# Kernel tuning notes

Hardware: AMD Instinct MI355X
Metric: run time of the kernel (lower is better)

Reference implementation:

```python
import jax, jax.numpy as jnp
import numpy as np

N, F_IN, HID, CLUST = 4096, 128, 128, 128
HEADS = 2
RADIUS = 2.0
TOPK_ADD = 2
MOTIF_TOPK = 8
ETA = 0.5
L0_GAMMA, L0_ZETA = -0.1, 1.1
NEG_SLOPE = 0.2
BN_EPS = 1e-5
NEG_INF = -1e9


def _row_topk(A, k):
    # keep top-k per row, symmetrize by max, zero diagonal (matches row_topk)
    n = A.shape[0]
    if n <= k:
        S = A
    else:
        vals, idx = jax.lax.top_k(A, k)
        S = jnp.zeros_like(A).at[jnp.arange(n)[:, None], idx].set(vals)
        S = jnp.maximum(S, S.T)
    return S * (1.0 - jnp.eye(n, dtype=A.dtype))


def _bn_eval(x, g, b, m, v):
    return (x - m) * g * jax.lax.rsqrt(v + BN_EPS) + b


def _gate(logits, tau):
    # hard-concrete gate, eval path
    t = jnp.clip(tau, 0.1, None)
    s = jax.nn.sigmoid(logits / t) * (L0_ZETA - L0_GAMMA) + L0_GAMMA
    return jnp.clip(s, 0.0, 1.0)


def _gcn_dense(feat, A_w, W, b):
    # GCN: D^-1/2 A D^-1/2 (X W) + b, zero-degree rows -> 0
    deg = A_w.sum(axis=1)
    dinv = jnp.where(deg > 0, jax.lax.rsqrt(jnp.where(deg > 0, deg, 1.0)), 0.0)
    An = dinv[:, None] * A_w * dinv[None, :]
    return An @ (feat @ W) + b


def setup_inputs():
    key = jax.random.key(0)
    ks = jax.random.split(key, 30)
    eye = jnp.eye(N, dtype=jnp.float32)
    p = 16.0 / N  # ~16 avg degree
    B = jax.random.uniform(ks[0], (N, N)) < p
    A_in = ((B | B.T) & ~jnp.eye(N, dtype=bool)).astype(jnp.float32)
    Mw = jnp.where(jax.random.uniform(ks[1], (N, N)) < p, jax.random.uniform(ks[2], (N, N)), 0.0)
    A_motif = jnp.maximum(Mw, Mw.T) * (1.0 - eye)
    coords = jax.random.randint(ks[3], (N, 2), 0, 64).astype(jnp.float32)
    x = jax.random.normal(ks[4], (N, F_IN))
    s_in = 1.0 / np.sqrt(F_IN)
    s_h = 1.0 / np.sqrt(2 * HID)
    return {
        'x': x, 'A_in': A_in, 'A_motif': A_motif, 'coords': coords,
        'gat_w': jax.random.normal(ks[5], (F_IN, HEADS * HID)) * s_in,
        'gat_asrc': jax.random.normal(ks[6], (HEADS, HID)) * s_h,
        'gat_adst': jax.random.normal(ks[7], (HEADS, HID)) * s_h,
        'gat_b': jnp.zeros((HEADS * HID,)),
        'bnA_g': jnp.ones((2 * HID,)), 'bnA_b': jnp.zeros((2 * HID,)),
        'bnA_m': jax.random.normal(ks[8], (2 * HID,)) * 0.1,
        'bnA_v': 0.5 + jax.random.uniform(ks[9], (2 * HID,)),
        'gcnM_w': jax.random.normal(ks[10], (F_IN, 2 * HID)) * s_in,
        'gcnM_b': jnp.zeros((2 * HID,)),
        'bnM_g': jnp.ones((2 * HID,)), 'bnM_b': jnp.zeros((2 * HID,)),
        'bnM_m': jax.random.normal(ks[11], (2 * HID,)) * 0.1,
        'bnM_v': 0.5 + jax.random.uniform(ks[12], (2 * HID,)),
        'mu': jnp.asarray(-3.0), 'tau': jnp.asarray(1.0),
        'prune_w': jax.random.normal(ks[13], (4 * HID + 1,)) * s_h,
        'prune_b': jnp.asarray(0.0),
        'rewire_w': jax.random.normal(ks[14], (4 * HID + 1,)) * s_h,
        'rewire_b': jnp.asarray(0.0),
        'pool_w': jax.random.normal(ks[15], (2 * HID, CLUST)) * s_h,
        'pool_b': jnp.zeros((CLUST,)),
    }


def reference(x, A_in, A_motif, coords, gat_w, gat_asrc, gat_adst, gat_b,
              bnA_g, bnA_b, bnA_m, bnA_v, gcnM_w, gcnM_b, bnM_g, bnM_b, bnM_m, bnM_v,
              mu, tau, prune_w, prune_b, rewire_w, rewire_b, pool_w, pool_b):
    n = x.shape[0]
    eye = jnp.eye(n, dtype=x.dtype)
    # --- GAT branch on A_in (dense masked attention; PyG adds self loops) ---
    Wx = (x @ gat_w).reshape(n, HEADS, HID)           # [N, heads, H]
    a_src = (Wx * gat_asrc).sum(-1)                   # [N, heads]
    a_dst = (Wx * gat_adst).sum(-1)
    e = jax.nn.leaky_relu(a_dst[:, None, :] + a_src[None, :, :], NEG_SLOPE)  # e[i,j,h]
    adj_mask = (A_in > 0) | jnp.eye(n, dtype=bool)
    e = jnp.where(adj_mask[..., None], e, NEG_INF)
    alpha = jax.nn.softmax(e, axis=1)                 # softmax over sources j
    h_A = jnp.einsum('ijh,jhd->ihd', alpha, Wx).reshape(n, HEADS * HID) + gat_b
    h_A = jax.nn.elu(_bn_eval(h_A, bnA_g, bnA_b, bnA_m, bnA_v))
    # --- motif branch ---
    M_hat = _row_topk(A_motif, MOTIF_TOPK)
    h_M = jax.nn.elu(_bn_eval(_gcn_dense(x, M_hat, gcnM_w, gcnM_b), bnM_g, bnM_b, bnM_m, bnM_v))
    h = h_A + jax.nn.softplus(mu) * h_M               # [N, 2H]
    d2 = 2 * HID
    triu = jnp.triu(jnp.ones((n, n), dtype=bool), 1)
    # --- prune gate on existing upper-tri edges (Linear is separable) ---
    pu = h @ prune_w[:d2]
    pv = h @ prune_w[d2:2 * d2]
    prune_logits = pu[:, None] + pv[None, :] + prune_w[2 * d2] * M_hat + prune_b
    z_prune = _gate(prune_logits, tau)
    edge_u = triu & (A_in > 0)
    Wp = jnp.where(edge_u, z_prune * A_in, 0.0)
    A_pruned = Wp + Wp.T
    # --- rewire candidates: L1 cdist within radius, non-edges, upper tri ---
    dist = jnp.abs(coords[:, None, :] - coords[None, :, :]).sum(-1)
    cand_u = (dist > 0) & (dist <= RADIUS) & (A_in < 1e-6) & triu
    ru = h @ rewire_w[:d2]
    rv = h @ rewire_w[d2:2 * d2]
    rew_logits = ru[:, None] + rv[None, :] + rewire_w[2 * d2] * M_hat + rewire_b
    Zu = jnp.where(cand_u, _gate(rew_logits, tau), 0.0)
    # per-node top-k selection over incident candidates (symmetric view)
    cand_sym = cand_u | cand_u.T
    scores = jnp.where(cand_sym, Zu + Zu.T, NEG_INF)
    thr = jax.lax.top_k(scores, TOPK_ADD)[0][:, -1]
    keep = (scores >= thr[:, None]) & cand_sym
    pair_keep = (keep | keep.T) & cand_u
    A_added_u = jnp.where(pair_keep, Zu, 0.0)
    A_added_sym = jnp.maximum(A_added_u, A_added_u.T)
    A_refined = A_pruned + ETA * A_added_sym
    # --- pooling GCN (default GCNConv adds self loops, weight 1) ---
    S = jax.nn.softmax(_gcn_dense(h, A_refined + eye, pool_w, pool_b), axis=1)  # [N, C]
    X_coarse = S.T @ h                                 # [C, 2H]
    A_c = S.T @ A_refined @ S
    A_c = A_c * (1.0 - jnp.eye(A_c.shape[0], dtype=A_c.dtype))
    A_coarse = _row_topk(A_c, MOTIF_TOPK)
    return X_coarse, A_coarse
```

## Files before the change

kernel.cpp:

```cpp
#include <hip/hip_runtime.h>
#include <hip/hip_bf16.h>
#include <stdint.h>

#define N 4096
#define FIN 128
#define HID 128
#define D2 256
#define CLUST 128
#define NEG_INF (-1e9f)
#define KAJ 128
#define KM 96
#define KC 64
#define KA (KAJ + KC)
#define CCAP 32
#define JCH 128
#define NCH (N/JCH)
#define CTILE 16
#define POSCAP 256

typedef __hip_bfloat16 bf16;

__device__ __forceinline__ float cvt(float v){ return v; }
__device__ __forceinline__ float cvt(bf16 v){ return __bfloat162float(v); }
__device__ __forceinline__ void stout(float* p, size_t i, float v){ p[i] = v; }
__device__ __forceinline__ void stout(bf16* p, size_t i, float v){ p[i] = __float2bfloat16(v); }

__device__ __forceinline__ float hc_gate(float l, float tau){
  float t = fmaxf(tau, 0.1f);
  float s = 1.f / (1.f + expf(-l / t));
  s = s * 1.2f - 0.1f;
  return fminf(fmaxf(s, 0.f), 1.f);
}

__global__ void k_detect(const void* x, const void* w, int* flag, int* cellCnt){
  __shared__ int hits;
  int t = threadIdx.x;
  if (t == 0) hits = 0;
  for (int i = t; i < 4096; i += 256) cellCnt[i] = 0;
  __syncthreads();
  const bf16* xb = (const bf16*)x;
  const bf16* wb = (const bf16*)w;
  int h = 0;
  for (int i = t; i < 2048; i += 256){
    float a = __bfloat162float(xb[i]);
    float b = __bfloat162float(wb[i]);
    if (!(fabsf(a) < 1e6f)) ++h;
    if (!(fabsf(b) < 1e6f)) ++h;
  }
  atomicAdd(&hits, h);
  __syncthreads();
  if (t == 0) *flag = (hits > 0) ? 1 : 0;
}

template<typename T>
__device__ void xw2_body(const T* x, const T* gat_w, const T* gcnM_w,
                         float* Wx, float* xwM, float* xr){
  int i0 = blockIdx.x * 4, t = threadIdx.x;
  for (int idx = t; idx < 4*FIN; idx += 256) xr[idx] = cvt(x[(size_t)i0*FIN + idx]);
  __syncthreads();
  float wx[4], xm[4];
  #pragma unroll
  for (int r = 0; r < 4; ++r){ wx[r] = 0.f; xm[r] = 0.f; }
  #pragma unroll 4
  for (int k = 0; k < FIN; ++k){
    float wa = cvt(gat_w[k*D2 + t]);
    float wm = cvt(gcnM_w[k*D2 + t]);
    #pragma unroll
    for (int r = 0; r < 4; ++r){
      wx[r] += xr[r*FIN + k] * wa;
      xm[r] += xr[r*FIN + k] * wm;
    }
  }
  #pragma unroll
  for (int r = 0; r < 4; ++r){
    Wx[(size_t)(i0+r)*D2 + t] = wx[r];
    xwM[(size_t)(i0+r)*D2 + t] = xm[r];
  }
}
__global__ void k_xw2(const int* fl, const void* x, const void* gw, const void* gmw,
                      float* Wx, float* xwM){
  __shared__ float xr[4*FIN];
  if (*fl) xw2_body<float>((const float*)x,(const float*)gw,(const float*)gmw,Wx,xwM,xr);
  else     xw2_body<bf16 >((const bf16*)x,(const bf16*)gw,(const bf16*)gmw,Wx,xwM,xr);
}

template<typename T>
__device__ void att_body(const float* Wx, const T* asrc, const T* adst,
                         float* a_src, float* a_dst){
  int w = threadIdx.x >> 6, l = threadIdx.x & 63;
  int row = blockIdx.x*4 + w;
  const float4* wr = (const float4*)(Wx + (size_t)row*D2);
  float4 v = wr[l];
  float s0 = cvt(asrc[l*4])*v.x + cvt(asrc[l*4+1])*v.y
           + cvt(asrc[l*4+2])*v.z + cvt(asrc[l*4+3])*v.w;
  float s1 = cvt(adst[l*4])*v.x + cvt(adst[l*4+1])*v.y
           + cvt(adst[l*4+2])*v.z + cvt(adst[l*4+3])*v.w;
  for (int d = 16; d > 0; d >>= 1){
    s0 += __shfl_down(s0, d, 32);
    s1 += __shfl_down(s1, d, 32);
  }
  if ((l & 31) == 0){
    a_src[row*2 + (l >> 5)] = s0;
    a_dst[row*2 + (l >> 5)] = s1;
  }
}
__global__ void k_att(const int* fl, const float* Wx, const void* as, const void* ad,
                      float* a_src, float* a_dst){
  if (*fl) att_body<float>(Wx,(const float*)as,(const float*)ad,a_src,a_dst);
  else     att_body<bf16 >(Wx,(const bf16*)as,(const bf16*)ad,a_src,a_dst);
}

__device__ __forceinline__ void t8_insert(unsigned long long* keys, float v, int j){
  unsigned long long key =
    ((unsigned long long)__float_as_uint(v) << 32) | (unsigned int)(~(unsigned int)j);
  if (key > keys[7]){
    keys[7] = key;
    #pragma unroll
    for (int q = 7; q > 0; --q){
      if (keys[q] > keys[q-1]){ unsigned long long tmp = keys[q]; keys[q] = keys[q-1]; keys[q-1] = tmp; }
    }
  }
}
__global__ void k_top8(const int* fl, const void* Amot, float* t8v, int* t8i,
                       int* Midx, float* Mval, int* Mcnt){
  __shared__ int pj[POSCAP];
  __shared__ float pv[POSCAP];
  __shared__ int cnt;
  int i = blockIdx.x, t = threadIdx.x;
  if (t == 0) cnt = 0;
  __syncthreads();
  if (*fl){
    const float4* rowp = (const float4*)((const float*)Amot + (size_t)i*N);
    for (int s = 0; s < N/1024; ++s){
      float4 v4 = rowp[s*256 + t];
      int jb = s*1024 + t*4;
      if (v4.x > 0.f){ int p = atomicAdd(&cnt,1); if (p < POSCAP){ pj[p] = jb;   pv[p] = v4.x; } }
      if (v4.y > 0.f){ int p = atomicAdd(&cnt,1); if (p < POSCAP){ pj[p] = jb+1; pv[p] = v4.y; } }
      if (v4.z > 0.f){ int p = atomicAdd(&cnt,1); if (p < POSCAP){ pj[p] = jb+2; pv[p] = v4.z; } }
      if (v4.w > 0.f){ int p = atomicAdd(&cnt,1); if (p < POSCAP){ pj[p] = jb+3; pv[p] = v4.w; } }
    }
  } else {
    const bf16* rowp = (const bf16*)Amot + (size_t)i*N;
    for (int j = t; j < N; j += 256){
      float v = cvt(rowp[j]);
      if (v > 0.f){ int p = atomicAdd(&cnt,1); if (p < POSCAP){ pj[p] = j; pv[p] = v; } }
    }
  }
  __syncthreads();
  if (t == 0){
    int n = min(cnt, POSCAP);
    unsigned long long keys[8];
    #pragma unroll
    for (int q = 0; q < 8; ++q) keys[q] = 0ull;
    for (int e = 0; e < n; ++e) t8_insert(keys, pv[e], pj[e]);
    int c = 0;
    #pragma unroll
    for (int r = 0; r < 8; ++r){
      float v = __uint_as_float((unsigned int)(keys[r] >> 32));
      int j = (int)(~(unsigned int)keys[r]);
      bool ok = (keys[r] != 0ull) && (v > 0.f);
      t8v[i*8 + r] = ok ? v : 0.f;
      t8i[i*8 + r] = ok ? j : -1;
      if (ok){ Midx[i*KM + c] = j; Mval[i*KM + c] = v; ++c; }
    }
    Mcnt[i] = c;
  }
}

__global__ void k_mscat(const float* __restrict__ t8v, const int* __restrict__ t8i,
                        int* __restrict__ Midx, float* __restrict__ Mval,
                        int* __restrict__ Mcnt){
  int e = blockIdx.x*256 + threadIdx.x;
  if (e >= N*8) return;
  int i = e >> 3;
  int j = t8i[e];
  if (j < 0) return;
  #pragma unroll
  for (int s = 0; s < 8; ++s) if (t8i[j*8 + s] == i) return;
  int p = atomicAdd(&Mcnt[j], 1);
  if (p < KM){ Midx[j*KM + p] = i; Mval[j*KM + p] = t8v[e]; }
}

__global__ void k_degM(const float* __restrict__ Mval, const int* __restrict__ Mcnt,
                       float* __restrict__ dinvM){
  int i = blockIdx.x*256 + threadIdx.x;
  if (i >= N) return;
  int n = min(Mcnt[i], KM);
  float s = 0.f;
  for (int e = 0; e < n; ++e) s += Mval[i*KM + e];
  dinvM[i] = (s > 0.f) ? rsqrtf(s) : 0.f;
}

template<typename T>
__device__ void motif_body(const int* Midx, const float* Mval, const int* Mcnt,
                           const float* dinvM, const float* xwM, const T* gcnM_b,
                           const T* bng, const T* bnb, const T* bnm, const T* bnv,
                           float* hM, int* nj, float* nw){
  int i = blockIdx.x, t = threadIdx.x;
  int n = min(Mcnt[i], KM);
  for (int e = t; e < n; e += 256){
    int j = Midx[i*KM + e];
    nj[e] = j;
    nw[e] = Mval[i*KM + e] * dinvM[j];
  }
  __syncthreads();
  float a0 = 0.f, a1 = 0.f, a2 = 0.f, a3 = 0.f;
  int e = 0;
  for (; e + 3 < n; e += 4){
    a0 += nw[e]   * xwM[nj[e]*D2 + t];
    a1 += nw[e+1] * xwM[nj[e+1]*D2 + t];
    a2 += nw[e+2] * xwM[nj[e+2]*D2 + t];
    a3 += nw[e+3] * xwM[nj[e+3]*D2 + t];
  }
  for (; e < n; ++e) a0 += nw[e] * xwM[nj[e]*D2 + t];
  float acc = (a0 + a1) + (a2 + a3);
  float val = acc * dinvM[i] + cvt(gcnM_b[t]);
  val = (val - cvt(bnm[t])) * cvt(bng[t]) * rsqrtf(cvt(bnv[t]) + 1e-5f) + cvt(bnb[t]);
  val = (val > 0.f) ? val : expm1f(val);
  hM[i*D2 + t] = val;
}
__global__ void k_motif_agg(const int* fl, const int* Midx, const float* Mval,
                            const int* Mcnt, const float* dinvM, const float* xwM,
                            const void* gb, const void* g, const void* b,
                            const void* m, const void* v, float* hM){
  __shared__ int nj[KM];
  __shared__ float nw[KM];
  if (*fl) motif_body<float>(Midx,Mval,Mcnt,dinvM,xwM,(const float*)gb,(const float*)g,
                             (const float*)b,(const float*)m,(const float*)v,hM,nj,nw);
  else     motif_body<bf16 >(Midx,Mval,Mcnt,dinvM,xwM,(const bf16*)gb,(const bf16*)g,
                             (const bf16*)b,(const bf16*)m,(const bf16*)v,hM,nj,nw);
}

__global__ void k_adj(const int* fl, const void* Ain,
                      int* __restrict__ AdjIdx, float* __restrict__ AdjVal,
                      int* __restrict__ AdjCnt){
  __shared__ int cnt;
  int i = blockIdx.x, t = threadIdx.x;
  if (t == 0) cnt = 0;
  __syncthreads();
  if (*fl){
    const float4* rowp = (const float4*)((const float*)Ain + (size_t)i*N);
    for (int s = 0; s < N/1024; ++s){
      float4 v4 = rowp[s*256 + t];
      int jb = s*1024 + t*4;
      if (v4.x > 0.f && jb   != i){ int p = atomicAdd(&cnt,1); if (p < KAJ){ AdjIdx[i*KAJ+p] = jb;   AdjVal[i*KAJ+p] = v4.x; } }
      if (v4.y > 0.f && jb+1 != i){ int p = atomicAdd(&cnt,1); if (p < KAJ){ AdjIdx[i*KAJ+p] = jb+1; AdjVal[i*KAJ+p] = v4.y; } }
      if (v4.z > 0.f && jb+2 != i){ int p = atomicAdd(&cnt,1); if (p < KAJ){ AdjIdx[i*KAJ+p] = jb+2; AdjVal[i*KAJ+p] = v4.z; } }
      if (v4.w > 0.f && jb+3 != i){ int p = atomicAdd(&cnt,1); if (p < KAJ){ AdjIdx[i*KAJ+p] = jb+3; AdjVal[i*KAJ+p] = v4.w; } }
    }
  } else {
    const bf16* rowp = (const bf16*)Ain + (size_t)i*N;
    for (int j = t; j < N; j += 256){
      float v = cvt(rowp[j]);
      if (v > 0.f && j != i){ int p = atomicAdd(&cnt,1); if (p < KAJ){ AdjIdx[i*KAJ+p] = j; AdjVal[i*KAJ+p] = v; } }
    }
  }
  __syncthreads();
  if (t == 0) AdjCnt[i] = min(cnt, KAJ);
}

template<typename T>
__device__ void gat_body(const int* AdjIdx, const int* AdjCnt, const float* Wx,
                         const float* a_src, const float* a_dst, const T* gat_b,
                         const T* bng, const T* bnb, const T* bnm, const T* bnv,
                         const float* hM, const T* mu,
                         float* h, int* nbr, float* ew, float* mm, float* inv){
  int i = blockIdx.x, t = threadIdx.x;
  int na = AdjCnt[i];
  for (int e = t; e < na; e += 256) nbr[e] = AdjIdx[i*KAJ + e];
  if (t == 0) nbr[na] = i;
  __syncthreads();
  int n = na + 1;
  float ad0 = a_dst[i*2], ad1 = a_dst[i*2 + 1];
  for (int e = t; e < n; e += 256){
    int j = nbr[e];
    float e0 = ad0 + a_src[j*2];
    float e1 = ad1 + a_src[j*2 + 1];
    e0 = (e0 > 0.f) ? e0 : 0.2f * e0;
    e1 = (e1 > 0.f) ? e1 : 0.2f * e1;
    ew[2*e] = e0; ew[2*e + 1] = e1;
  }
  __syncthreads();
  if (t == 0){
    float m0 = -3.4e38f, m1 = -3.4e38f;
    for (int e = 0; e < n; ++e){ m0 = fmaxf(m0, ew[2*e]); m1 = fmaxf(m1, ew[2*e+1]); }
    mm[0] = m0; mm[1] = m1;
  }
  __syncthreads();
  for (int e = t; e < n; e += 256){
    ew[2*e]   = expf(ew[2*e]   - mm[0]);
    ew[2*e+1] = expf(ew[2*e+1] - mm[1]);
  }
  __syncthreads();
  if (t == 0){
    float s0 = 0.f, s1 = 0.f;
    for (int e = 0; e < n; ++e){ s0 += ew[2*e]; s1 += ew[2*e+1]; }
    inv[0] = 1.f/s0; inv[1] = 1.f/s1;
  }
  __syncthreads();
  int hh = t >> 7;
  float a0 = 0.f, a1 = 0.f, a2 = 0.f, a3 = 0.f;
  int e = 0;
  for (; e + 3 < n; e += 4){
    a0 += ew[2*e + hh]     * Wx[nbr[e]*D2 + t];
    a1 += ew[2*(e+1) + hh] * Wx[nbr[e+1]*D2 + t];
    a2 += ew[2*(e+2) + hh] * Wx[nbr[e+2]*D2 + t];
    a3 += ew[2*(e+3) + hh] * Wx[nbr[e+3]*D2 + t];
  }
  for (; e < n; ++e) a0 += ew[2*e + hh] * Wx[nbr[e]*D2 + t];
  float acc = (a0 + a1) + (a2 + a3);
  float val = acc * inv[hh] + cvt(gat_b[t]);
  val = (val - cvt(bnm[t])) * cvt(bng[t]) * rsqrtf(cvt(bnv[t]) + 1e-5f) + cvt(bnb[t]);
  val = (val > 0.f) ? val : expm1f(val);
  float spmu = log1pf(expf(cvt(mu[0])));
  h[i*D2 + t] = val + spmu * hM[i*D2 + t];
}
__global__ void k_gat_agg(const int* fl, const int* AdjIdx, const int* AdjCnt,
                          const float* Wx, const float* a_src, const float* a_dst,
                          const void* gb, const void* g, const void* b, const void* m,
                          const void* v, const float* hM, const void* mu, float* h){
  __shared__ int nbr[KAJ + 1];
  __shared__ float ew[(KAJ + 1)*2];
  __shared__ float mm[2], inv[2];
  if (*fl) gat_body<float>(AdjIdx,AdjCnt,Wx,a_src,a_dst,(const float*)gb,(const float*)g,
                           (const float*)b,(const float*)m,(const float*)v,hM,(const float*)mu,
                           h,nbr,ew,mm,inv);
  else     gat_body<bf16 >(AdjIdx,AdjCnt,Wx,a_src,a_dst,(const bf16*)gb,(const bf16*)g,
                           (const bf16*)b,(const bf16*)m,(const bf16*)v,hM,(const bf16*)mu,
                           h,nbr,ew,mm,inv);
}

template<typename T>
__device__ void puv_body(const float* h, const T* pw, const T* rw,
                         float* pu, float* pv, float* ru, float* rv, float* red){
  int i = blockIdx.x, t = threadIdx.x;
  float hv = h[i*D2 + t];
  float v0 = hv * cvt(pw[t]);
  float v1 = hv * cvt(pw[D2 + t]);
  float v2 = hv * cvt(rw[t]);
  float v3 = hv * cvt(rw[D2 + t]);
  red[t] = v0; __syncthreads();
  for (int k = 128; k > 0; k >>= 1){ if (t < k) red[t] += red[t+k]; __syncthreads(); }
  if (t == 0) pu[i] = red[0];
  __syncthreads();
  red[t] = v1; __syncthreads();
  for (int k = 128; k > 0; k >>= 1){ if (t < k) red[t] += red[t+k]; __syncthreads(); }
  if (t == 0) pv[i] = red[0];
  __syncthreads();
  red[t] = v2; __syncthreads();
  for (int k = 128; k > 0; k >>= 1){ if (t < k) red[t] += red[t+k]; __syncthreads(); }
  if (t == 0) ru[i] = red[0];
  __syncthreads();
  red[t] = v3; __syncthreads();
  for (int k = 128; k > 0; k >>= 1){ if (t < k) red[t] += red[t+k]; __syncthreads(); }
  if (t == 0) rv[i] = red[0];
}
__global__ void k_puv(const int* fl, const float* h, const void* pw, const void* rw,
                      float* pu, float* pv, float* ru, float* rv){
  __shared__ float red[256];
  if (*fl) puv_body<float>(h,(const float*)pw,(const float*)rw,pu,pv,ru,rv,red);
  else     puv_body<bf16 >(h,(const bf16*)pw,(const bf16*)rw,pu,pv,ru,rv,red);
}

template<typename T>
__device__ void gridb_body(const T* coords, int* cellCnt, int* cellNode){
  int i = blockIdx.x*256 + threadIdx.x;
  if (i >= N) return;
  int cx = (int)cvt(coords[2*i]), cy = (int)cvt(coords[2*i+1]);
  int cell = cy*64 + cx;
  int p = atomicAdd(&cellCnt[cell], 1);
  if (p < CCAP) cellNode[cell*CCAP + p] = i;
}
__global__ void k_gridb(const int* fl, const void* coords, int* cellCnt, int* cellNode){
  if (*fl) gridb_body<float>((const float*)coords, cellCnt, cellNode);
  else     gridb_body<bf16 >((const bf16*)coords, cellCnt, cellNode);
}

template<typename T>
__device__ void cand_body(const T* coords, const T* Ain,
                          const int* Midx, const float* Mval, const int* Mcnt,
                          const int* cellCnt, const int* cellNode,
                          const float* ru, const float* rv,
                          const T* rw, const T* rb, const T* taup,
                          int* Cidx, float* Cz, int* Ccnt, float* thr,
                          int* scI, float* scZ, int* scn){
  int w = threadIdx.x >> 6, l = threadIdx.x & 63;
  int i = blockIdx.x*4 + w;
  if (l == 0) scn[w] = 0;
  __syncthreads();
  float cix = cvt(coords[2*i]), ciy = cvt(coords[2*i+1]);
// ... 230 lines not shown
    float acc[CTILE];
    #pragma unroll
    for (int cc = 0; cc < CTILE; ++cc) acc[cc] = 0.f;
    for (int j = 0; j < JCH; ++j){
      float v = T_[(size_t)(j0 + j)*CLUST + tt];
      #pragma unroll
      for (int cc = 0; cc < CTILE; ++cc) acc[cc] += ss[j][cc] * v;
    }
    #pragma unroll
    for (int cc = 0; cc < CTILE; ++cc)
      PA[((size_t)ch*CLUST + c0 + cc)*CLUST + tt] = acc[cc];
  }
}

template<typename OT>
__device__ void coarse2_body(const float* PX, const float* PA, OT* Xout, float* Ac){
  int c = blockIdx.x, t = threadIdx.x;
  if (t < 256){
    float s = 0.f;
    #pragma unroll 8
    for (int ch = 0; ch < NCH; ++ch) s += PX[((size_t)ch*CLUST + c)*D2 + t];
    stout(Xout, (size_t)c*D2 + t, s);
  } else {
    int tt = t - 256;
    float s = 0.f;
    #pragma unroll 8
    for (int ch = 0; ch < NCH; ++ch) s += PA[((size_t)ch*CLUST + c)*CLUST + tt];
    Ac[c*CLUST + tt] = (tt == c) ? 0.f : s;
  }
}
__global__ void k_coarse2(const int* fl, const float* PX, const float* PA,
                          void* out, float* Ac){
  if (*fl) coarse2_body<float>(PX, PA, (float*)out, Ac);
  else     coarse2_body<bf16 >(PX, PA, (bf16*)out, Ac);
}

__global__ void k_top8c(const float* __restrict__ Ac, float* __restrict__ Acs){
  __shared__ unsigned long long red[128];
  int r = blockIdx.x, t = threadIdx.x;
  float v = Ac[r*CLUST + t];
  unsigned long long mykey =
    ((unsigned long long)__float_as_uint(fmaxf(v, 0.f)) << 32) | (unsigned int)(~(unsigned int)t);
  unsigned long long last = ~0ull;
  bool selected = false;
  for (int q = 0; q < 8; ++q){
    red[t] = (mykey < last) ? mykey : 0ull;
    __syncthreads();
    for (int k = 64; k > 0; k >>= 1){
      if (t < k){ if (red[t+k] > red[t]) red[t] = red[t+k]; }
      __syncthreads();
    }
    unsigned long long win = red[0];
    __syncthreads();
    if (win != 0ull && win == mykey) selected = true;
    last = win;
  }
  Acs[r*CLUST + t] = (selected && v > 0.f) ? v : 0.f;
}

template<typename OT>
__device__ void sym_body(const float* Acs, OT* out){
  int r = blockIdx.x, t = threadIdx.x;
  float v = (r == t) ? 0.f : fmaxf(Acs[r*CLUST + t], Acs[t*CLUST + r]);
  stout(out, (size_t)(CLUST*D2) + r*CLUST + t, v);
}
__global__ void k_sym(const int* fl, const float* Acs, void* out){
  if (*fl) sym_body<float>(Acs, (float*)out);
  else     sym_body<bf16 >(Acs, (bf16*)out);
}

extern "C" void kernel_launch(void* const* d_in, const int* in_sizes, int n_in,
                              void* d_out, int out_size, void* d_ws, size_t ws_size,
// ... 31 lines not shown
    void* r = (void*)p;
    p += (bytes + 255) & ~(size_t)255;
    return r;
  };
  int*   flag    = (int*)  alloc(256);
  float* Wx      = (float*)alloc((size_t)N*D2*4);
  float* xwM     = (float*)alloc((size_t)N*D2*4);
  float* a_src   = (float*)alloc((size_t)N*2*4);
  float* a_dst   = (float*)alloc((size_t)N*2*4);
  float* t8v     = (float*)alloc((size_t)N*8*4);
  int*   t8i     = (int*)  alloc((size_t)N*8*4);
  int*   Midx    = (int*)  alloc((size_t)N*KM*4);
  float* Mval    = (float*)alloc((size_t)N*KM*4);
  int*   Mcnt    = (int*)  alloc((size_t)N*4);
  float* dinvM   = (float*)alloc((size_t)N*4);
  float* hM      = (float*)alloc((size_t)N*D2*4);
  float* hbuf    = (float*)alloc((size_t)N*D2*4);
  float* pu      = (float*)alloc((size_t)N*4);
  float* pv      = (float*)alloc((size_t)N*4);
  float* ru      = (float*)alloc((size_t)N*4);
  float* rv      = (float*)alloc((size_t)N*4);
  int*   AdjIdx  = (int*)  alloc((size_t)N*KAJ*4);
  float* AdjVal  = (float*)alloc((size_t)N*KAJ*4);
  int*   AdjCnt  = (int*)  alloc((size_t)N*4);
  int*   cellCnt = (int*)  alloc((size_t)4096*4);
  int*   cellNode= (int*)  alloc((size_t)4096*CCAP*4);
  int*   Cidx    = (int*)  alloc((size_t)N*KC*4);
  float* Cz      = (float*)alloc((size_t)N*KC*4);
  int*   Ccnt    = (int*)  alloc((size_t)N*4);
  float* thr     = (float*)alloc((size_t)N*4);
  int*   Aidx    = (int*)  alloc((size_t)N*KA*4);
  float* Aval    = (float*)alloc((size_t)N*KA*4);
  int*   Acnt    = (int*)  alloc((size_t)N*4);
  float* dinvR   = (float*)alloc((size_t)N*4);
  float* hW      = (float*)alloc((size_t)N*CLUST*4);
  float* S       = (float*)alloc((size_t)N*CLUST*4);
  float* T       = (float*)alloc((size_t)N*CLUST*4);
  float* PX      = (float*)alloc((size_t)NCH*CLUST*D2*4);
  float* PA      = (float*)alloc((size_t)NCH*CLUST*CLUST*4);
  float* Ac      = (float*)alloc((size_t)CLUST*CLUST*4);
  float* Acs     = (float*)alloc((size_t)CLUST*CLUST*4);

  k_detect<<<1, 256, 0, stream>>>(x, gat_w, flag, cellCnt);
  k_xw2<<<N/4, 256, 0, stream>>>(flag, x, gat_w, gcnM_w, Wx, xwM);
  k_att<<<N/4, 256, 0, stream>>>(flag, Wx, gat_asrc, gat_adst, a_src, a_dst);
  k_top8<<<N, 256, 0, stream>>>(flag, A_motif, t8v, t8i, Midx, Mval, Mcnt);
  k_mscat<<<(N*8)/256, 256, 0, stream>>>(t8v, t8i, Midx, Mval, Mcnt);
  k_degM<<<N/256, 256, 0, stream>>>(Mval, Mcnt, dinvM);
  k_motif_agg<<<N, 256, 0, stream>>>(flag, Midx, Mval, Mcnt, dinvM, xwM, gcnM_b,
                                     bnM_g, bnM_b, bnM_m, bnM_v, hM);
  k_adj<<<N, 256, 0, stream>>>(flag, A_in, AdjIdx, AdjVal, AdjCnt);
  k_gridb<<<16, 256, 0, stream>>>(flag, coords, cellCnt, cellNode);
  k_gat_agg<<<N, 256, 0, stream>>>(flag, AdjIdx, AdjCnt, Wx, a_src, a_dst, gat_b,
                                   bnA_g, bnA_b, bnA_m, bnA_v, hM, mu, hbuf);
  k_puv<<<N, 256, 0, stream>>>(flag, hbuf, prune_w, rewire_w, pu, pv, ru, rv);
  k_cand<<<N/4, 256, 0, stream>>>(flag, coords, A_in, Midx, Mval, Mcnt, cellCnt, cellNode,
                                  ru, rv, rewire_w, rewire_b, tau, Cidx, Cz, Ccnt, thr);
  k_aref<<<N/4, 256, 0, stream>>>(flag, AdjIdx, AdjVal, AdjCnt, Midx, Mval, Mcnt,
                                  pu, pv, prune_w, prune_b, tau, Cidx, Cz, Ccnt, thr,
                                  Aidx, Aval, Acnt, dinvR);
  k_hw<<<N/8, 128, 0, stream>>>(flag, hbuf, pool_w, hW);
  k_preS<<<N, 256, 0, stream>>>(flag, Aidx, Aval, Acnt, dinvR, hW, pool_b, S);
  k_T<<<N, 256, 0, stream>>>(Aidx, Aval, Acnt, S, T);
  k_coarse1<<<dim3(CLUST/CTILE, NCH), 384, 0, stream>>>(S, hbuf, T, PX, PA);
  k_coarse2<<<CLUST, 384, 0, stream>>>(flag, PX, PA, d_out, Ac);
  k_top8c<<<CLUST, 128, 0, stream>>>(Ac, Acs);
  k_sym<<<CLUST, 128, 0, stream>>>(flag, Acs, d_out);
}
```

Baseline: 404.1 us.

## Fuse kernels: xw2+att, motif/adj/grid scans, motif+GAT+puv aggregation, coarse2+top8

Merges several small launches into larger kernels. The attention dot products are computed from shared memory inside the x@W kernel, and the A_motif and A_in row scans plus grid bucketing share one pass per row. The motif GCN, GAT aggregation and prune/rewire projections run in one per-node kernel, which drops the hM intermediate buffer. The coarse top-8 selection moves into k_coarse2 as a serial insertion by one thread. This cuts launch overhead and global round-trips, at the cost of larger per-block work and a serial top-8 on a single thread.

```diff
diff --git a/kernel.cpp b/kernel.cpp
--- a/kernel.cpp
+++ b/kernel.cpp
@@ -32,6 +32,18 @@
   return fminf(fmaxf(s, 0.f), 1.f);
 }
 
+__device__ __forceinline__ void t8_insert(unsigned long long* keys, float v, int j){
+  unsigned long long key =
+    ((unsigned long long)__float_as_uint(v) << 32) | (unsigned int)(~(unsigned int)j);
+  if (key > keys[7]){
+    keys[7] = key;
+    #pragma unroll
+    for (int q = 7; q > 0; --q){
+      if (keys[q] > keys[q-1]){ unsigned long long tmp = keys[q]; keys[q] = keys[q-1]; keys[q-1] = tmp; }
+    }
+  }
+}
+
 __global__ void k_detect(const void* x, const void* w, int* flag, int* cellCnt){
   __shared__ int hits;
   int t = threadIdx.x;
@@ -54,9 +66,11 @@
 
 template<typename T>
 __device__ void xw2_body(const T* x, const T* gat_w, const T* gcnM_w,
-                         float* Wx, float* xwM, float* xr){
+                         const T* asrc, const T* adst,
+                         float* Wx, float* xwM, float* a_src, float* a_dst,
+                         float* sh){
   int i0 = blockIdx.x * 4, t = threadIdx.x;
-  for (int idx = t; idx < 4*FIN; idx += 256) xr[idx] = cvt(x[(size_t)i0*FIN + idx]);
+  for (int idx = t; idx < 4*FIN; idx += 256) sh[idx] = cvt(x[(size_t)i0*FIN + idx]);
   __syncthreads();
   float wx[4], xm[4];
   #pragma unroll
@@ -67,8 +81,8 @@
     float wm = cvt(gcnM_w[k*D2 + t]);
     #pragma unroll
     for (int r = 0; r < 4; ++r){
-      wx[r] += xr[r*FIN + k] * wa;
-      xm[r] += xr[r*FIN + k] * wm;
+      wx[r] += sh[r*FIN + k] * wa;
+      xm[r] += sh[r*FIN + k] * wm;
     }
   }
   #pragma unroll
@@ -76,21 +90,13 @@
     Wx[(size_t)(i0+r)*D2 + t] = wx[r];
     xwM[(size_t)(i0+r)*D2 + t] = xm[r];
   }
-}
-__global__ void k_xw2(const int* fl, const void* x, const void* gw, const void* gmw,
-                      float* Wx, float* xwM){
-  __shared__ float xr[4*FIN];
-  if (*fl) xw2_body<float>((const float*)x,(const float*)gw,(const float*)gmw,Wx,xwM,xr);
-  else     xw2_body<bf16 >((const bf16*)x,(const bf16*)gw,(const bf16*)gmw,Wx,xwM,xr);
-}
-
-template<typename T>
-__device__ void att_body(const float* Wx, const T* asrc, const T* adst,
-                         float* a_src, float* a_dst){
-  int w = threadIdx.x >> 6, l = threadIdx.x & 63;
-  int row = blockIdx.x*4 + w;
-  const float4* wr = (const float4*)(Wx + (size_t)row*D2);
-  float4 v = wr[l];
+  __syncthreads();
+  #pragma unroll
+  for (int r = 0; r < 4; ++r) sh[r*256 + t] = wx[r];
+  __syncthreads();
+  int w = t >> 6, l = t & 63;
+  int row = i0 + w;
+  float4 v = ((const float4*)(sh + w*256))[l];
   float s0 = cvt(asrc[l*4])*v.x + cvt(asrc[l*4+1])*v.y
            + cvt(asrc[l*4+2])*v.z + cvt(asrc[l*4+3])*v.w;
   float s1 = cvt(adst[l*4])*v.x + cvt(adst[l*4+1])*v.y
@@ -104,51 +110,52 @@
     a_dst[row*2 + (l >> 5)] = s1;
   }
 }
-__global__ void k_att(const int* fl, const float* Wx, const void* as, const void* ad,
-                      float* a_src, float* a_dst){
-  if (*fl) att_body<float>(Wx,(const float*)as,(const float*)ad,a_src,a_dst);
-  else     att_body<bf16 >(Wx,(const bf16*)as,(const bf16*)ad,a_src,a_dst);
-}
-
-__device__ __forceinline__ void t8_insert(unsigned long long* keys, float v, int j){
-  unsigned long long key =
-    ((unsigned long long)__float_as_uint(v) << 32) | (unsigned int)(~(unsigned int)j);
-  if (key > keys[7]){
-    keys[7] = key;
-    #pragma unroll
-    for (int q = 7; q > 0; --q){
-      if (keys[q] > keys[q-1]){ unsigned long long tmp = keys[q]; keys[q] = keys[q-1]; keys[q-1] = tmp; }
-    }
-  }
-}
-__global__ void k_top8(const int* fl, const void* Amot, float* t8v, int* t8i,
-                       int* Midx, float* Mval, int* Mcnt){
-  __shared__ int pj[POSCAP];
-  __shared__ float pv[POSCAP];
-  __shared__ int cnt;
+__global__ void k_xw2(const int* fl, const void* x, const void* gw, const void* gmw,
+                      const void* as, const void* ad,
+                      float* Wx, float* xwM, float* a_src, float* a_dst){
+  __shared__ float sh[1024];
+  if (*fl) xw2_body<float>((const float*)x,(const float*)gw,(const float*)gmw,
+                           (const float*)as,(const float*)ad,Wx,xwM,a_src,a_dst,sh);
+  else     xw2_body<bf16 >((const bf16*)x,(const bf16*)gw,(const bf16*)gmw,
+                           (const bf16*)as,(const bf16*)ad,Wx,xwM,a_src,a_dst,sh);
+}
+
+template<typename T>
+__device__ void scan_body(const T* Amot, const T* Ain, const T* coords,
+                          float* t8v, int* t8i, int* Midx, float* Mval, int* Mcnt,
+                          int* AdjIdx, float* AdjVal, int* AdjCnt,
+                          int* cellCnt, int* cellNode,
+                          int* pj, float* pv, int* cntM, int* cntA){
   int i = blockIdx.x, t = threadIdx.x;
-  if (t == 0) cnt = 0;
-  __syncthreads();
-  if (*fl){
-    const float4* rowp = (const float4*)((const float*)Amot + (size_t)i*N);
-    for (int s = 0; s < N/1024; ++s){
-      float4 v4 = rowp[s*256 + t];
-      int jb = s*1024 + t*4;
-      if (v4.x > 0.f){ int p = atomicAdd(&cnt,1); if (p < POSCAP){ pj[p] = jb;   pv[p] = v4.x; } }
-      if (v4.y > 0.f){ int p = atomicAdd(&cnt,1); if (p < POSCAP){ pj[p] = jb+1; pv[p] = v4.y; } }
-      if (v4.z > 0.f){ int p = atomicAdd(&cnt,1); if (p < POSCAP){ pj[p] = jb+2; pv[p] = v4.z; } }
-      if (v4.w > 0.f){ int p = atomicAdd(&cnt,1); if (p < POSCAP){ pj[p] = jb+3; pv[p] = v4.w; } }
-    }
-  } else {
-    const bf16* rowp = (const bf16*)Amot + (size_t)i*N;
+  if (t == 0){
+    *cntM = 0; *cntA = 0;
+    int cx = (int)cvt(coords[2*i]), cy = (int)cvt(coords[2*i+1]);
+    int cell = cy*64 + cx;
+    int p = atomicAdd(&cellCnt[cell], 1);
+    if (p < CCAP) cellNode[cell*CCAP + p] = i;
+  }
+  __syncthreads();
+  {
+    const T* rowp = Amot + (size_t)i*N;
     for (int j = t; j < N; j += 256){
       float v = cvt(rowp[j]);
-      if (v > 0.f){ int p = atomicAdd(&cnt,1); if (p < POSCAP){ pj[p] = j; pv[p] = v; } }
+      if (v > 0.f){ int p = atomicAdd(cntM,1); if (p < POSCAP){ pj[p] = j; pv[p] = v; } }
+    }
+  }
+  {
+    const T* rowp = Ain + (size_t)i*N;
+    for (int j = t; j < N; j += 256){
+      float v = cvt(rowp[j]);
+      if (v > 0.f && j != i){
+        int p = atomicAdd(cntA,1);
+        if (p < KAJ){ AdjIdx[i*KAJ+p] = j; AdjVal[i*KAJ+p] = v; }
+      }
     }
   }
   __syncthreads();
   if (t == 0){
-    int n = min(cnt, POSCAP);
+    AdjCnt[i] = min(*cntA, KAJ);
+    int n = min(*cntM, POSCAP);
     unsigned long long keys[8];
     #pragma unroll
     for (int q = 0; q < 8; ++q) keys[q] = 0ull;
@@ -165,6 +172,77 @@
     }
     Mcnt[i] = c;
   }
+}
+__device__ void scan_body_f4(const float* Amot, const float* Ain, const float* coords,
+                             float* t8v, int* t8i, int* Midx, float* Mval, int* Mcnt,
+                             int* AdjIdx, float* AdjVal, int* AdjCnt,
+                             int* cellCnt, int* cellNode,
+                             int* pj, float* pv, int* cntM, int* cntA){
+  int i = blockIdx.x, t = threadIdx.x;
+  if (t == 0){
+    *cntM = 0; *cntA = 0;
+    int cx = (int)coords[2*i], cy = (int)coords[2*i+1];
+    int cell = cy*64 + cx;
+    int p = atomicAdd(&cellCnt[cell], 1);
+    if (p < CCAP) cellNode[cell*CCAP + p] = i;
+  }
+  __syncthreads();
+  {
+    const float4* rowp = (const float4*)(Amot + (size_t)i*N);
+    for (int s = 0; s < N/1024; ++s){
+      float4 v4 = rowp[s*256 + t];
+      int jb = s*1024 + t*4;
+      if (v4.x > 0.f){ int p = atomicAdd(cntM,1); if (p < POSCAP){ pj[p] = jb;   pv[p] = v4.x; } }
+      if (v4.y > 0.f){ int p = atomicAdd(cntM,1); if (p < POSCAP){ pj[p] = jb+1; pv[p] = v4.y; } }
+      if (v4.z > 0.f){ int p = atomicAdd(cntM,1); if (p < POSCAP){ pj[p] = jb+2; pv[p] = v4.z; } }
+      if (v4.w > 0.f){ int p = atomicAdd(cntM,1); if (p < POSCAP){ pj[p] = jb+3; pv[p] = v4.w; } }
+    }
+  }
+  {
+    const float4* rowp = (const float4*)(Ain + (size_t)i*N);
+    for (int s = 0; s < N/1024; ++s){
+      float4 v4 = rowp[s*256 + t];
+      int jb = s*1024 + t*4;
+      if (v4.x > 0.f && jb   != i){ int p = atomicAdd(cntA,1); if (p < KAJ){ AdjIdx[i*KAJ+p] = jb;   AdjVal[i*KAJ+p] = v4.x; } }
+      if (v4.y > 0.f && jb+1 != i){ int p = atomicAdd(cntA,1); if (p < KAJ){ AdjIdx[i*KAJ+p] = jb+1; AdjVal[i*KAJ+p] = v4.y; } }
+      if (v4.z > 0.f && jb+2 != i){ int p = atomicAdd(cntA,1); if (p < KAJ){ AdjIdx[i*KAJ+p] = jb+2; AdjVal[i*KAJ+p] = v4.z; } }
+      if (v4.w > 0.f && jb+3 != i){ int p = atomicAdd(cntA,1); if (p < KAJ){ AdjIdx[i*KAJ+p] = jb+3; AdjVal[i*KAJ+p] = v4.w; } }
+    }
+  }
+  __syncthreads();
+  if (t == 0){
+    AdjCnt[i] = min(*cntA, KAJ);
+    int n = min(*cntM, POSCAP);
+    unsigned long long keys[8];
+    #pragma unroll
+    for (int q = 0; q < 8; ++q) keys[q] = 0ull;
+    for (int e = 0; e < n; ++e) t8_insert(keys, pv[e], pj[e]);
+    int c = 0;
+    #pragma unroll
+    for (int r = 0; r < 8; ++r){
+      float v = __uint_as_float((unsigned int)(keys[r] >> 32));
+      int j = (int)(~(unsigned int)keys[r]);
+      bool ok = (keys[r] != 0ull) && (v > 0.f);
+      t8v[i*8 + r] = ok ? v : 0.f;
+      t8i[i*8 + r] = ok ? j : -1;
+      if (ok){ Midx[i*KM + c] = j; Mval[i*KM + c] = v; ++c; }
+    }
+    Mcnt[i] = c;
+  }
+}
+__global__ void k_scan(const int* fl, const void* Amot, const void* Ain, const void* coords,
+                       float* t8v, int* t8i, int* Midx, float* Mval, int* Mcnt,
+                       int* AdjIdx, float* AdjVal, int* AdjCnt,
+                       int* cellCnt, int* cellNode){
+  __shared__ int pj[POSCAP];
+  __shared__ float pv[POSCAP];
+  __shared__ int cntM, cntA;
+  if (*fl) scan_body_f4((const float*)Amot,(const float*)Ain,(const float*)coords,
+                        t8v,t8i,Midx,Mval,Mcnt,AdjIdx,AdjVal,AdjCnt,cellCnt,cellNode,
+                        pj,pv,&cntM,&cntA);
+  else     scan_body<bf16>((const bf16*)Amot,(const bf16*)Ain,(const bf16*)coords,
+                        t8v,t8i,Midx,Mval,Mcnt,AdjIdx,AdjVal,AdjCnt,cellCnt,cellNode,
+                        pj,pv,&cntM,&cntA);
 }
 
 __global__ void k_mscat(const float* __restrict__ t8v, const int* __restrict__ t8i,
@@ -192,115 +270,70 @@
 }
 
 template<typename T>
-__device__ void motif_body(const int* Midx, const float* Mval, const int* Mcnt,
-                           const float* dinvM, const float* xwM, const T* gcnM_b,
-                           const T* bng, const T* bnb, const T* bnm, const T* bnv,
-                           float* hM, int* nj, float* nw){
+__device__ void fuse_body(const int* Midx, const float* Mval, const int* Mcnt,
+                          const float* dinvM, const float* xwM,
+                          const int* AdjIdx, const int* AdjCnt, const float* Wx,
+                          const float* a_src, const float* a_dst,
+                          const T* gcnM_b, const T* bMg, const T* bMb, const T* bMm, const T* bMv,
+                          const T* gat_b, const T* bAg, const T* bAb, const T* bAm, const T* bAv,
+                          const T* mu, const T* pw, const T* rw,
+                          float* h, float* pu, float* pv, float* ru, float* rv,
+                          int* nj, float* nw, int* nbr, float* ew,
+                          float* mm, float* inv, float* part){
   int i = blockIdx.x, t = threadIdx.x;
-  int n = min(Mcnt[i], KM);
-  for (int e = t; e < n; e += 256){
+  int nm = min(Mcnt[i], KM);
+  for (int e = t; e < nm; e += 256){
     int j = Midx[i*KM + e];
     nj[e] = j;
     nw[e] = Mval[i*KM + e] * dinvM[j];
   }
+  int na = AdjCnt[i];
+  for (int e = t; e < na; e += 256) nbr[e] = AdjIdx[i*KAJ + e];
+  if (t == 0) nbr[na] = i;
   __syncthreads();
   float a0 = 0.f, a1 = 0.f, a2 = 0.f, a3 = 0.f;
   int e = 0;
-  for (; e + 3 < n; e += 4){
+  for (; e + 3 < nm; e += 4){
     a0 += nw[e]   * xwM[nj[e]*D2 + t];
     a1 += nw[e+1] * xwM[nj[e+1]*D2 + t];
     a2 += nw[e+2] * xwM[nj[e+2]*D2 + t];
     a3 += nw[e+3] * xwM[nj[e+3]*D2 + t];
   }
-  for (; e < n; ++e) a0 += nw[e] * xwM[nj[e]*D2 + t];
-  float acc = (a0 + a1) + (a2 + a3);
-  float val = acc * dinvM[i] + cvt(gcnM_b[t]);
-  val = (val - cvt(bnm[t])) * cvt(bng[t]) * rsqrtf(cvt(bnv[t]) + 1e-5f) + cvt(bnb[t]);
-  val = (val > 0.f) ? val : expm1f(val);
-  hM[i*D2 + t] = val;
-}
-__global__ void k_motif_agg(const int* fl, const int* Midx, const float* Mval,
-                            const int* Mcnt, const float* dinvM, const float* xwM,
-                            const void* gb, const void* g, const void* b,
-                            const void* m, const void* v, float* hM){
-  __shared__ int nj[KM];
-  __shared__ float nw[KM];
-  if (*fl) motif_body<float>(Midx,Mval,Mcnt,dinvM,xwM,(const float*)gb,(const float*)g,
-                             (const float*)b,(const float*)m,(const float*)v,hM,nj,nw);
-  else     motif_body<bf16 >(Midx,Mval,Mcnt,dinvM,xwM,(const bf16*)gb,(const bf16*)g,
-                             (const bf16*)b,(const bf16*)m,(const bf16*)v,hM,nj,nw);
-}
-
-__global__ void k_adj(const int* fl, const void* Ain,
-                      int* __restrict__ AdjIdx, float* __restrict__ AdjVal,
-                      int* __restrict__ AdjCnt){
-  __shared__ int cnt;
-  int i = blockIdx.x, t = threadIdx.x;
-  if (t == 0) cnt = 0;
-  __syncthreads();
-  if (*fl){
-    const float4* rowp = (const float4*)((const float*)Ain + (size_t)i*N);
-    for (int s = 0; s < N/1024; ++s){
-      float4 v4 = rowp[s*256 + t];
-      int jb = s*1024 + t*4;
-      if (v4.x > 0.f && jb   != i){ int p = atomicAdd(&cnt,1); if (p < KAJ){ AdjIdx[i*KAJ+p] = jb;   AdjVal[i*KAJ+p] = v4.x; } }
-      if (v4.y > 0.f && jb+1 != i){ int p = atomicAdd(&cnt,1); if (p < KAJ){ AdjIdx[i*KAJ+p] = jb+1; AdjVal[i*KAJ+p] = v4.y; } }
-      if (v4.z > 0.f && jb+2 != i){ int p = atomicAdd(&cnt,1); if (p < KAJ){ AdjIdx[i*KAJ+p] = jb+2; AdjVal[i*KAJ+p] = v4.z; } }
-      if (v4.w > 0.f && jb+3 != i){ int p = atomicAdd(&cnt,1); if (p < KAJ){ AdjIdx[i*KAJ+p] = jb+3; AdjVal[i*KAJ+p] = v4.w; } }
-    }
-  } else {
-    const bf16* rowp = (const bf16*)Ain + (size_t)i*N;
-    for (int j = t; j < N; j += 256){
-      float v = cvt(rowp[j]);
-      if (v > 0.f && j != i){ int p = atomicAdd(&cnt,1); if (p < KAJ){ AdjIdx[i*KAJ+p] = j; AdjVal[i*KAJ+p] = v; } }
-    }
-  }
-  __syncthreads();
-  if (t == 0) AdjCnt[i] = min(cnt, KAJ);
-}
-
-template<typename T>
-__device__ void gat_body(const int* AdjIdx, const int* AdjCnt, const float* Wx,
-                         const float* a_src, const float* a_dst, const T* gat_b,
-                         const T* bng, const T* bnb, const T* bnm, const T* bnv,
-                         const float* hM, const T* mu,
-                         float* h, int* nbr, float* ew, float* mm, float* inv){
-  int i = blockIdx.x, t = threadIdx.x;
-  int na = AdjCnt[i];
-  for (int e = t; e < na; e += 256) nbr[e] = AdjIdx[i*KAJ + e];
-  if (t == 0) nbr[na] = i;
-  __syncthreads();
+  for (; e < nm; ++e) a0 += nw[e] * xwM[nj[e]*D2 + t];
+  float hMt = ((a0 + a1) + (a2 + a3)) * dinvM[i] + cvt(gcnM_b[t]);
+  hMt = (hMt - cvt(bMm[t])) * cvt(bMg[t]) * rsqrtf(cvt(bMv[t]) + 1e-5f) + cvt(bMb[t]);
+  hMt = (hMt > 0.f) ? hMt : expm1f(hMt);
   int n = na + 1;
   float ad0 = a_dst[i*2], ad1 = a_dst[i*2 + 1];
-  for (int e = t; e < n; e += 256){
-    int j = nbr[e];
+  for (int q = t; q < n; q += 256){
+    int j = nbr[q];
     float e0 = ad0 + a_src[j*2];
     float e1 = ad1 + a_src[j*2 + 1];
     e0 = (e0 > 0.f) ? e0 : 0.2f * e0;
     e1 = (e1 > 0.f) ? e1 : 0.2f * e1;
-    ew[2*e] = e0; ew[2*e + 1] = e1;
+    ew[2*q] = e0; ew[2*q + 1] = e1;
   }
   __syncthreads();
   if (t == 0){
     float m0 = -3.4e38f, m1 = -3.4e38f;
-    for (int e = 0; e < n; ++e){ m0 = fmaxf(m0, ew[2*e]); m1 = fmaxf(m1, ew[2*e+1]); }
+    for (int q = 0; q < n; ++q){ m0 = fmaxf(m0, ew[2*q]); m1 = fmaxf(m1, ew[2*q+1]); }
     mm[0] = m0; mm[1] = m1;
   }
   __syncthreads();
-  for (int e = t; e < n; e += 256){
-    ew[2*e]   = expf(ew[2*e]   - mm[0]);
-    ew[2*e+1] = expf(ew[2*e+1] - mm[1]);
+  for (int q = t; q < n; q += 256){
+    ew[2*q]   = expf(ew[2*q]   - mm[0]);
+    ew[2*q+1] = expf(ew[2*q+1] - mm[1]);
   }
   __syncthreads();
   if (t == 0){
     float s0 = 0.f, s1 = 0.f;
-    for (int e = 0; e < n; ++e){ s0 += ew[2*e]; s1 += ew[2*e+1]; }
+    for (int q = 0; q < n; ++q){ s0 += ew[2*q]; s1 += ew[2*q+1]; }
     inv[0] = 1.f/s0; inv[1] = 1.f/s1;
   }
   __syncthreads();
   int hh = t >> 7;
-  float a0 = 0.f, a1 = 0.f, a2 = 0.f, a3 = 0.f;
-  int e = 0;
+  a0 = a1 = a2 = a3 = 0.f;
+  e = 0;
   for (; e + 3 < n; e += 4){
     a0 += ew[2*e + hh]     * Wx[nbr[e]*D2 + t];
     a1 += ew[2*(e+1) + hh] * Wx[nbr[e+1]*D2 + t];
@@ -308,72 +341,65 @@
     a3 += ew[2*(e+3) + hh] * Wx[nbr[e+3]*D2 + t];
   }
   for (; e < n; ++e) a0 += ew[2*e + hh] * Wx[nbr[e]*D2 + t];
-  float acc = (a0 + a1) + (a2 + a3);
-  float val = acc * inv[hh] + cvt(gat_b[t]);
-  val = (val - cvt(bnm[t])) * cvt(bng[t]) * rsqrtf(cvt(bnv[t]) + 1e-5f) + cvt(bnb[t]);
+  float val = ((a0 + a1) + (a2 + a3)) * inv[hh] + cvt(gat_b[t]);
+  val = (val - cvt(bAm[t])) * cvt(bAg[t]) * rsqrtf(cvt(bAv[t]) + 1e-5f) + cvt(bAb[t]);
   val = (val > 0.f) ? val : expm1f(val);
   float spmu = log1pf(expf(cvt(mu[0])));
-  h[i*D2 + t] = val + spmu * hM[i*D2 + t];
-}
-__global__ void k_gat_agg(const int* fl, const int* AdjIdx, const int* AdjCnt,
-                          const float* Wx, const float* a_src, const float* a_dst,
-                          const void* gb, const void* g, const void* b, const void* m,
-                          const void* v, const float* hM, const void* mu, float* h){
+  float ht = val + spmu * hMt;
+  h[i*D2 + t] = ht;
+  float v0 = ht * cvt(pw[t]);
+  float v1 = ht * cvt(pw[D2 + t]);
+  float v2 = ht * cvt(rw[t]);
+  float v3 = ht * cvt(rw[D2 + t]);
+  for (int d = 32; d > 0; d >>= 1){
+    v0 += __shfl_down(v0, d, 64);
+    v1 += __shfl_down(v1, d, 64);
+    v2 += __shfl_down(v2, d, 64);
+    v3 += __shfl_down(v3, d, 64);
+  }
+  int w = t >> 6;
+  if ((t & 63) == 0){
+    part[w*4]   = v0; part[w*4+1] = v1;
+    part[w*4+2] = v2; part[w*4+3] = v3;
+  }
+  __syncthreads();
+  if (t == 0){
+    pu[i] = (part[0]  + part[4])  + (part[8]  + part[12]);
+    pv[i] = (part[1]  + part[5])  + (part[9]  + part[13]);
+    ru[i] = (part[2]  + part[6])  + (part[10] + part[14]);
+    rv[i] = (part[3]  + part[7])  + (part[11] + part[15]);
+  }
+}
+__global__ void k_fuse_agg(const int* fl, const int* Midx, const float* Mval,
+                           const int* Mcnt, const float* dinvM, const float* xwM,
+                           const int* AdjIdx, const int* AdjCnt, const float* Wx,
+                           const float* a_src, const float* a_dst,
+                           const void* gmb, const void* bMg, const void* bMb,
+                           const void* bMm, const void* bMv,
+                           const void* gb, const void* bAg, const void* bAb,
+                           const void* bAm, const void* bAv,
+                           const void* mu, const void* pw, const void* rw,
+                           float* h, float* pu, float* pv, float* ru, float* rv){
+  __shared__ int nj[KM];
+  __shared__ float nw[KM];
   __shared__ int nbr[KAJ + 1];
   __shared__ float ew[(KAJ + 1)*2];
   __shared__ float mm[2], inv[2];
-  if (*fl) gat_body<float>(AdjIdx,AdjCnt,Wx,a_src,a_dst,(const float*)gb,(const float*)g,
-                           (const float*)b,(const float*)m,(const float*)v,hM,(const float*)mu,
-                           h,nbr,ew,mm,inv);
-  else     gat_body<bf16 >(AdjIdx,AdjCnt,Wx,a_src,a_dst,(const bf16*)gb,(const bf16*)g,
-                           (const bf16*)b,(const bf16*)m,(const bf16*)v,hM,(const bf16*)mu,
-                           h,nbr,ew,mm,inv);
-}
-
-template<typename T>
-__device__ void puv_body(const float* h, const T* pw, const T* rw,
-                         float* pu, float* pv, float* ru, float* rv, float* red){
-  int i = blockIdx.x, t = threadIdx.x;
-  float hv = h[i*D2 + t];
-  float v0 = hv * cvt(pw[t]);
-  float v1 = hv * cvt(pw[D2 + t]);
-  float v2 = hv * cvt(rw[t]);
-  float v3 = hv * cvt(rw[D2 + t]);
-  red[t] = v0; __syncthreads();
-  for (int k = 128; k > 0; k >>= 1){ if (t < k) red[t] += red[t+k]; __syncthreads(); }
-  if (t == 0) pu[i] = red[0];
-  __syncthreads();
-  red[t] = v1; __syncthreads();
-  for (int k = 128; k > 0; k >>= 1){ if (t < k) red[t] += red[t+k]; __syncthreads(); }
-  if (t == 0) pv[i] = red[0];
-  __syncthreads();
-  red[t] = v2; __syncthreads();
-  for (int k = 128; k > 0; k >>= 1){ if (t < k) red[t] += red[t+k]; __syncthreads(); }
-  if (t == 0) ru[i] = red[0];
-  __syncthreads();
-  red[t] = v3; __syncthreads();
-  for (int k = 128; k > 0; k >>= 1){ if (t < k) red[t] += red[t+k]; __syncthreads(); }
-  if (t == 0) rv[i] = red[0];
-}
-__global__ void k_puv(const int* fl, const float* h, const void* pw, const void* rw,
-                      float* pu, float* pv, float* ru, float* rv){
-  __shared__ float red[256];
-  if (*fl) puv_body<float>(h,(const float*)pw,(const float*)rw,pu,pv,ru,rv,red);
-  else     puv_body<bf16 >(h,(const bf16*)pw,(const bf16*)rw,pu,pv,ru,rv,red);
-}
-
-template<typename T>
-__device__ void gridb_body(const T* coords, int* cellCnt, int* cellNode){
-  int i = blockIdx.x*256 + threadIdx.x;
-  if (i >= N) return;
-  int cx = (int)cvt(coords[2*i]), cy = (int)cvt(coords[2*i+1]);
-  int cell = cy*64 + cx;
-  int p = atomicAdd(&cellCnt[cell], 1);
-  if (p < CCAP) cellNode[cell*CCAP + p] = i;
-}
-__global__ void k_gridb(const int* fl, const void* coords, int* cellCnt, int* cellNode){
-  if (*fl) gridb_body<float>((const float*)coords, cellCnt, cellNode);
-  else     gridb_body<bf16 >((const bf16*)coords, cellCnt, cellNode);
+  __shared__ float part[16];
+  if (*fl) fuse_body<float>(Midx,Mval,Mcnt,dinvM,xwM,AdjIdx,AdjCnt,Wx,a_src,a_dst,
+                            (const float*)gmb,(const float*)bMg,(const float*)bMb,
+                            (const float*)bMm,(const float*)bMv,
+                            (const float*)gb,(const float*)bAg,(const float*)bAb,
+                            (const float*)bAm,(const float*)bAv,
+                            (const float*)mu,(const float*)pw,(const float*)rw,
+                            h,pu,pv,ru,rv,nj,nw,nbr,ew,mm,inv,part);
+  else     fuse_body<bf16 >(Midx,Mval,Mcnt,dinvM,xwM,AdjIdx,AdjCnt,Wx,a_src,a_dst,
+                            (const bf16*)gmb,(const bf16*)bMg,(const bf16*)bMb,
+                            (const bf16*)bMm,(const bf16*)bMv,
+                            (const bf16*)gb,(const bf16*)bAg,(const bf16*)bAb,
+                            (const bf16*)bAm,(const bf16*)bAv,
+                            (const bf16*)mu,(const bf16*)pw,(const bf16*)rw,
+                            h,pu,pv,ru,rv,nj,nw,nbr,ew,mm,inv,part);
 }
 
 template<typename T>
@@ -634,7 +660,8 @@
 }
 
 template<typename OT>
-__device__ void coarse2_body(const float* PX, const float* PA, OT* Xout, float* Ac){
+__device__ void coarse2_body(const float* PX, const float* PA, OT* Xout, float* Acs,
+                             float* acr, unsigned long long* k8){
   int c = blockIdx.x, t = threadIdx.x;
   if (t < 256){
     float s = 0.f;
@@ -646,36 +673,35 @@
     float s = 0.f;
     #pragma unroll 8
     for (int ch = 0; ch < NCH; ++ch) s += PA[((size_t)ch*CLUST + c)*CLUST + tt];
-    Ac[c*CLUST + tt] = (tt == c) ? 0.f : s;
+    acr[tt] = (tt == c) ? 0.f : s;
+  }
+  __syncthreads();
+  if (t == 0){
+    unsigned long long keys[8];
+    #pragma unroll
+    for (int q = 0; q < 8; ++q) keys[q] = 0ull;
+    for (int j = 0; j < CLUST; ++j) t8_insert(keys, fmaxf(acr[j], 0.f), j);
+    #pragma unroll
+    for (int q = 0; q < 8; ++q) k8[q] = keys[q];
+  }
+  __syncthreads();
+  if (t >= 256){
+    int tt = t - 256;
+    float v = acr[tt];
+    unsigned long long mykey =
+      ((unsigned long long)__float_as_uint(fmaxf(v, 0.f)) << 32) | (unsigned int)(~(unsigned int)tt);
+    bool sel = false;
+    #pragma unroll
+    for (int q = 0; q < 8; ++q) if (k8[q] == mykey && k8[q] != 0ull) sel = true;
+    Acs[c*CLUST + tt] = (sel && v > 0.f) ? v : 0.f;
   }
 }
 __global__ void k_coarse2(const int* fl, const float* PX, const float* PA,
-                          void* out, float* Ac){
-  if (*fl) coarse2_body<float>(PX, PA, (float*)out, Ac);
-  else     coarse2_body<bf16 >(PX, PA, (bf16*)out, Ac);
-}
-
-__global__ void k_top8c(const float* __restrict__ Ac, float* __restrict__ Acs){
-  __shared__ unsigned long long red[128];
-  int r = blockIdx.x, t = threadIdx.x;
-  float v = Ac[r*CLUST + t];
-  unsigned long long mykey =
-    ((unsigned long long)__float_as_uint(fmaxf(v, 0.f)) << 32) | (unsigned int)(~(unsigned int)t);
-  unsigned long long last = ~0ull;
-  bool selected = false;
-  for (int q = 0; q < 8; ++q){
-    red[t] = (mykey < last) ? mykey : 0ull;
-    __syncthreads();
-    for (int k = 64; k > 0; k >>= 1){
-      if (t < k){ if (red[t+k] > red[t]) red[t] = red[t+k]; }
-      __syncthreads();
-    }
-    unsigned long long win = red[0];
-    __syncthreads();
-    if (win != 0ull && win == mykey) selected = true;
-    last = win;
-  }
-  Acs[r*CLUST + t] = (selected && v > 0.f) ? v : 0.f;
+                          void* out, float* Acs){
+  __shared__ float acr[CLUST];
+  __shared__ unsigned long long k8[8];
+  if (*fl) coarse2_body<float>(PX, PA, (float*)out, Acs, acr, k8);
+  else     coarse2_body<bf16 >(PX, PA, (bf16*)out, Acs, acr, k8);
 }
 
 template<typename OT>
@@ -737,7 +763,6 @@
   float* Mval    = (float*)alloc((size_t)N*KM*4);
   int*   Mcnt    = (int*)  alloc((size_t)N*4);
   float* dinvM   = (float*)alloc((size_t)N*4);
-  float* hM      = (float*)alloc((size_t)N*D2*4);
   float* hbuf    = (float*)alloc((size_t)N*D2*4);
   float* pu      = (float*)alloc((size_t)N*4);
   float* pv      = (float*)alloc((size_t)N*4);
@@ -761,22 +786,22 @@
   float* T       = (float*)alloc((size_t)N*CLUST*4);
   float* PX      = (float*)alloc((size_t)NCH*CLUST*D2*4);
   float* PA      = (float*)alloc((size_t)NCH*CLUST*CLUST*4);
-  float* Ac      = (float*)alloc((size_t)CLUST*CLUST*4);
   float* Acs     = (float*)alloc((size_t)CLUST*CLUST*4);
 
   k_detect<<<1, 256, 0, stream>>>(x, gat_w, flag, cellCnt);
-  k_xw2<<<N/4, 256, 0, stream>>>(flag, x, gat_w, gcnM_w, Wx, xwM);
-  k_att<<<N/4, 256, 0, stream>>>(flag, Wx, gat_asrc, gat_adst, a_src, a_dst);
-  k_top8<<<N, 256, 0, stream>>>(flag, A_motif, t8v, t8i, Midx, Mval, Mcnt);
+  k_xw2<<<N/4, 256, 0, stream>>>(flag, x, gat_w, gcnM_w, gat_asrc, gat_adst,
+                                 Wx, xwM, a_src, a_dst);
+  k_scan<<<N, 256, 0, stream>>>(flag, A_motif, A_in, coords, t8v, t8i,
+                                Midx, Mval, Mcnt, AdjIdx, AdjVal, AdjCnt,
+                                cellCnt, cellNode);
   k_mscat<<<(N*8)/256, 256, 0, stream>>>(t8v, t8i, Midx, Mval, Mcnt);
   k_degM<<<N/256, 256, 0, stream>>>(Mval, Mcnt, dinvM);
-  k_motif_agg<<<N, 256, 0, stream>>>(flag, Midx, Mval, Mcnt, dinvM, xwM, gcnM_b,
-                                     bnM_g, bnM_b, bnM_m, bnM_v, hM);
-  k_adj<<<N, 256, 0, stream>>>(flag, A_in, AdjIdx, AdjVal, AdjCnt);
-  k_gridb<<<16, 256, 0, stream>>>(flag, coords, cellCnt, cellNode);
-  k_gat_agg<<<N, 256, 0, stream>>>(flag, AdjIdx, AdjCnt, Wx, a_src, a_dst, gat_b,
-                                   bnA_g, bnA_b, bnA_m, bnA_v, hM, mu, hbuf);
-  k_puv<<<N, 256, 0, stream>>>(flag, hbuf, prune_w, rewire_w, pu, pv, ru, rv);
+  k_fuse_agg<<<N, 256, 0, stream>>>(flag, Midx, Mval, Mcnt, dinvM, xwM,
+                                    AdjIdx, AdjCnt, Wx, a_src, a_dst,
+                                    gcnM_b, bnM_g, bnM_b, bnM_m, bnM_v,
+                                    gat_b, bnA_g, bnA_b, bnA_m, bnA_v,
+                                    mu, prune_w, rewire_w,
+                                    hbuf, pu, pv, ru, rv);
   k_cand<<<N/4, 256, 0, stream>>>(flag, coords, A_in, Midx, Mval, Mcnt, cellCnt, cellNode,
                                   ru, rv, rewire_w, rewire_b, tau, Cidx, Cz, Ccnt, thr);
   k_aref<<<N/4, 256, 0, stream>>>(flag, AdjIdx, AdjVal, AdjCnt, Midx, Mval, Mcnt,
@@ -786,7 +811,6 @@
   k_preS<<<N, 256, 0, stream>>>(flag, Aidx, Aval, Acnt, dinvR, hW, pool_b, S);
   k_T<<<N, 256, 0, stream>>>(Aidx, Aval, Acnt, S, T);
   k_coarse1<<<dim3(CLUST/CTILE, NCH), 384, 0, stream>>>(S, hbuf, T, PX, PA);
-  k_coarse2<<<CLUST, 384, 0, stream>>>(flag, PX, PA, d_out, Ac);
-  k_top8c<<<CLUST, 128, 0, stream>>>(Ac, Acs);
+  k_coarse2<<<CLUST, 384, 0, stream>>>(flag, PX, PA, d_out, Acs);
   k_sym<<<CLUST, 128, 0, stream>>>(flag, Acs, d_out);
 }
```

Result: no change. 403.8 us (-0.1%).
